# Kernel optimization log

Measured on AMD Instinct MI355X. Metric: run time of the kernel, lower is better.

## Reference

```python
import jax, jax.numpy as jnp
import numpy as np

M, N_IN, K_OUT = 65536, 512, 512  # tokens, in_features, out_features


def setup_inputs() -> dict:
    key = jax.random.key(0)
    k1, k2, k3 = jax.random.split(key, 3)
    X = jax.random.normal(k1, (M, N_IN), dtype=jnp.float32)
    Weight = jax.random.normal(k2, (K_OUT, N_IN), dtype=jnp.float32) * 0.02
    Bias = jax.random.normal(k3, (K_OUT,), dtype=jnp.float32) * 0.02
    return {"X": X, "Weight": Weight, "Bias": Bias}


def reference(X, Weight, Bias):
    # Normalization constants (map X and W into (0,1)-ish analog ranges)
    n_x = jnp.max(X)
    n_w = jnp.maximum(jnp.abs(jnp.min(Weight)), jnp.abs(jnp.max(Weight)))
    X_norm = X / n_x
    W_norm = Weight / n_w
    # quick_split_W3D: W_norm = W_pos - W_neg, each non-negative
    W_pos = jax.nn.relu(W_norm)
    W_neg = jax.nn.relu(-W_norm)
    # Matmul_2D (SIMULATE='False' path): the (m,n,k) Hadamard-product expansion
    # summed over n is exactly X_norm @ W.T; compute the two GEMMs explicitly
    # to preserve the split-weight floating-point path.
    prod_plus = X_norm @ W_pos.T   # (m, k)
    prod_minus = X_norm @ W_neg.T  # (m, k)
    out = n_x * n_w * (prod_plus - prod_minus) + Bias
    return out
```

## Files before the change

### kernel.cpp

```cpp
#include <hip/hip_runtime.h>
#include <hip/hip_bf16.h>


typedef __bf16 bf16x8 __attribute__((ext_vector_type(8)));
typedef float  f32x4  __attribute__((ext_vector_type(4)));

constexpr int M_TOK = 65536;
constexpr int K_IN  = 512;
constexpr int N_OUT = 512;

constexpr int BM = 128, BN = 128, BK = 32;
constexpr int PK = BK + 8;

__global__ __launch_bounds__(256, 2)
void linear_sim_kernel(const float* __restrict__ X,
                       const float* __restrict__ W,
                       const float* __restrict__ Bias,
                       float* __restrict__ Out)
{
    __shared__ __bf16 As[BM][PK];
    __shared__ __bf16 Bs[BN][PK];

    const int bid = blockIdx.x;
    const int nb  = bid & 3;
    const int mb  = bid >> 2;
    const int m0 = mb * BM, n0 = nb * BN;

    const int tid  = threadIdx.x;
    const int lane = tid & 63;
    const int wave = tid >> 6;
    const int wm = wave >> 1;
    const int wn = wave & 1;

    const int srow = tid >> 1;
    const int sk   = (tid & 1) * 16;

    const float* Xp = X + (size_t)(m0 + srow) * K_IN + sk;
    const float* Wp = W + (size_t)(n0 + srow) * K_IN + sk;

    f32x4 acc[16];
    const f32x4 zero = {0.f, 0.f, 0.f, 0.f};
    #pragma unroll
    for (int i = 0; i < 16; ++i) acc[i] = zero;

    const int l15 = lane & 15;
    const int lg  = lane >> 4;

    for (int k0 = 0; k0 < K_IN; k0 += BK) {
        f32x4 xa[4], wb[4];
        #pragma unroll
        for (int q = 0; q < 4; ++q) xa[q] = *(const f32x4*)(Xp + k0 + q * 4);
        #pragma unroll
        for (int q = 0; q < 4; ++q) wb[q] = *(const f32x4*)(Wp + k0 + q * 4);

        __syncthreads();

        #pragma unroll
        for (int h = 0; h < 2; ++h) {
            bf16x8 ta, tb;
            #pragma unroll
            for (int q = 0; q < 2; ++q)
                #pragma unroll
                for (int e = 0; e < 4; ++e) {
                    ta[q * 4 + e] = (__bf16)xa[h * 2 + q][e];
                    tb[q * 4 + e] = (__bf16)wb[h * 2 + q][e];
                }
            *(bf16x8*)&As[srow][sk + h * 8] = ta;
            *(bf16x8*)&Bs[srow][sk + h * 8] = tb;
        }

        __syncthreads();

        bf16x8 af[4], bfr[4];
        #pragma unroll
        for (int i = 0; i < 4; ++i)
            af[i] = *(const bf16x8*)&As[wm * 64 + i * 16 + l15][lg * 8];
        #pragma unroll
        for (int i = 0; i < 4; ++i)
            bfr[i] = *(const bf16x8*)&Bs[wn * 64 + i * 16 + l15][lg * 8];

        #pragma unroll
        for (int mi = 0; mi < 4; ++mi)
            #pragma unroll
            for (int ni = 0; ni < 4; ++ni)
                acc[mi * 4 + ni] = __builtin_amdgcn_mfma_f32_16x16x32_bf16(
                    af[mi], bfr[ni], acc[mi * 4 + ni], 0, 0, 0);
    }

    #pragma unroll
    for (int ni = 0; ni < 4; ++ni) {
        const int col = n0 + wn * 64 + ni * 16 + l15;
        const float bv = Bias[col];
        #pragma unroll
        for (int mi = 0; mi < 4; ++mi) {
            const int row0 = m0 + wm * 64 + mi * 16 + lg * 4;
            f32x4 a = acc[mi * 4 + ni];
            #pragma unroll
            for (int r = 0; r < 4; ++r)
                Out[(size_t)(row0 + r) * N_OUT + col] = a[r] + bv;
        }
    }
}

extern "C" void kernel_launch(void* const* d_in, const int* in_sizes, int n_in,
                              void* d_out, int out_size, void* d_ws, size_t ws_size,
                              hipStream_t stream) {
    const float* X    = (const float*)d_in[0];
    const float* W    = (const float*)d_in[1];
    const float* Bias = (const float*)d_in[2];
    float* Out        = (float*)d_out;

    dim3 grid((M_TOK / BM) * (N_OUT / BN));
    linear_sim_kernel<<<grid, dim3(256), 0, stream>>>(X, W, Bias, Out);
}
```

Before: 305.9 us.

## Double-buffer LDS tiles with register prefetch, XCD-aware block remap, nontemporal stores

Splits the shared-memory tiles into two buffers. The next K-slice is loaded from global memory into registers and written into the alternate buffer after the MFMAs, which cuts the loop from two barriers per step to one and overlaps the loads with compute. It also raises the launch-bounds occupancy hint to 4 blocks per CU. Block indices are remapped so consecutive blocks are spread across XCDs, and the output is written with nontemporal stores. In exchange the LDS footprint doubles and register pressure rises, which could conflict with the higher occupancy target.

```diff
diff --git a/kernel.cpp b/kernel.cpp
--- a/kernel.cpp
+++ b/kernel.cpp
@@ -11,19 +11,21 @@
 
 constexpr int BM = 128, BN = 128, BK = 32;
 constexpr int PK = BK + 8;
+constexpr int NT = K_IN / BK;
 
-__global__ __launch_bounds__(256, 2)
+__global__ __launch_bounds__(256, 4)
 void linear_sim_kernel(const float* __restrict__ X,
                        const float* __restrict__ W,
                        const float* __restrict__ Bias,
                        float* __restrict__ Out)
 {
-    __shared__ __bf16 As[BM][PK];
-    __shared__ __bf16 Bs[BN][PK];
+    __shared__ __bf16 As[2][BM][PK];
+    __shared__ __bf16 Bs[2][BN][PK];
 
-    const int bid = blockIdx.x;
-    const int nb  = bid & 3;
-    const int mb  = bid >> 2;
+    const int d  = blockIdx.x;
+    const int o  = (d & 7) * 256 + (d >> 3);
+    const int nb = o & 3;
+    const int mb = o >> 2;
     const int m0 = mb * BM, n0 = nb * BN;
 
     const int tid  = threadIdx.x;
@@ -46,38 +48,44 @@
     const int l15 = lane & 15;
     const int lg  = lane >> 4;
 
-    for (int k0 = 0; k0 < K_IN; k0 += BK) {
-        f32x4 xa[4], wb[4];
+    f32x4 xa[4], wb[4];
+    #pragma unroll
+    for (int q = 0; q < 4; ++q) xa[q] = *(const f32x4*)(Xp + q * 4);
+    #pragma unroll
+    for (int q = 0; q < 4; ++q) wb[q] = *(const f32x4*)(Wp + q * 4);
+    #pragma unroll
+    for (int h = 0; h < 2; ++h) {
+        bf16x8 ta, tb;
         #pragma unroll
-        for (int q = 0; q < 4; ++q) xa[q] = *(const f32x4*)(Xp + k0 + q * 4);
-        #pragma unroll
-        for (int q = 0; q < 4; ++q) wb[q] = *(const f32x4*)(Wp + k0 + q * 4);
+        for (int q = 0; q < 2; ++q)
+            #pragma unroll
+            for (int e = 0; e < 4; ++e) {
+                ta[q * 4 + e] = (__bf16)xa[h * 2 + q][e];
+                tb[q * 4 + e] = (__bf16)wb[h * 2 + q][e];
+            }
+        *(bf16x8*)&As[0][srow][sk + h * 8] = ta;
+        *(bf16x8*)&Bs[0][srow][sk + h * 8] = tb;
+    }
+    __syncthreads();
 
-        __syncthreads();
-
-        #pragma unroll
-        for (int h = 0; h < 2; ++h) {
-            bf16x8 ta, tb;
+    int cur = 0;
+    for (int t = 0; t < NT; ++t) {
+        const bool pf = (t + 1 < NT);
+        if (pf) {
+            const int k0 = (t + 1) * BK;
             #pragma unroll
-            for (int q = 0; q < 2; ++q)
-                #pragma unroll
-                for (int e = 0; e < 4; ++e) {
-                    ta[q * 4 + e] = (__bf16)xa[h * 2 + q][e];
-                    tb[q * 4 + e] = (__bf16)wb[h * 2 + q][e];
-                }
-            *(bf16x8*)&As[srow][sk + h * 8] = ta;
-            *(bf16x8*)&Bs[srow][sk + h * 8] = tb;
+            for (int q = 0; q < 4; ++q) xa[q] = *(const f32x4*)(Xp + k0 + q * 4);
+            #pragma unroll
+            for (int q = 0; q < 4; ++q) wb[q] = *(const f32x4*)(Wp + k0 + q * 4);
         }
-
-        __syncthreads();
 
         bf16x8 af[4], bfr[4];
         #pragma unroll
         for (int i = 0; i < 4; ++i)
-            af[i] = *(const bf16x8*)&As[wm * 64 + i * 16 + l15][lg * 8];
+            af[i] = *(const bf16x8*)&As[cur][wm * 64 + i * 16 + l15][lg * 8];
         #pragma unroll
         for (int i = 0; i < 4; ++i)
-            bfr[i] = *(const bf16x8*)&Bs[wn * 64 + i * 16 + l15][lg * 8];
+            bfr[i] = *(const bf16x8*)&Bs[cur][wn * 64 + i * 16 + l15][lg * 8];
 
         #pragma unroll
         for (int mi = 0; mi < 4; ++mi)
@@ -85,6 +93,24 @@
             for (int ni = 0; ni < 4; ++ni)
                 acc[mi * 4 + ni] = __builtin_amdgcn_mfma_f32_16x16x32_bf16(
                     af[mi], bfr[ni], acc[mi * 4 + ni], 0, 0, 0);
+
+        if (pf) {
+            #pragma unroll
+            for (int h = 0; h < 2; ++h) {
+                bf16x8 ta, tb;
+                #pragma unroll
+                for (int q = 0; q < 2; ++q)
+                    #pragma unroll
+                    for (int e = 0; e < 4; ++e) {
+                        ta[q * 4 + e] = (__bf16)xa[h * 2 + q][e];
+                        tb[q * 4 + e] = (__bf16)wb[h * 2 + q][e];
+                    }
+                *(bf16x8*)&As[cur ^ 1][srow][sk + h * 8] = ta;
+                *(bf16x8*)&Bs[cur ^ 1][srow][sk + h * 8] = tb;
+            }
+        }
+        __syncthreads();
+        cur ^= 1;
     }
 
     #pragma unroll
@@ -97,7 +123,8 @@
             f32x4 a = acc[mi * 4 + ni];
             #pragma unroll
             for (int r = 0; r < 4; ++r)
-                Out[(size_t)(row0 + r) * N_OUT + col] = a[r] + bv;
+                __builtin_nontemporal_store(a[r] + bv,
+                    &Out[(size_t)(row0 + r) * N_OUT + col]);
         }
     }
 }
```

Result: slower. 328.4 us (+7.4%).

## Stage X tiles via async global-to-LDS loads with double buffering and swizzle

Applied to the files above, without the earlier changes.

Replaces the register-staged bf16 shared-memory tiles with fp32 X tiles copied directly into LDS by global_load_lds, double-buffered so the next tile's copy overlaps the current tile's MFMA work. An XOR swizzle on chunk positions avoids LDS bank conflicts. Weight fragments are now loaded straight from global memory into registers, skipping LDS. The block index is remapped for L2 locality and occupancy is raised to 3 blocks per CU. The trade-offs are a larger fp32 LDS footprint, bf16 conversion on the read side, and redundant weight loads per wave that lean on the cache.

```diff
diff --git a/kernel.cpp b/kernel.cpp
--- a/kernel.cpp
+++ b/kernel.cpp
@@ -10,74 +10,93 @@
 constexpr int N_OUT = 512;
 
 constexpr int BM = 128, BN = 128, BK = 32;
-constexpr int PK = BK + 8;
+constexpr int NT = K_IN / BK;
 
-__global__ __launch_bounds__(256, 2)
+__global__ __launch_bounds__(256, 3)
 void linear_sim_kernel(const float* __restrict__ X,
                        const float* __restrict__ W,
                        const float* __restrict__ Bias,
                        float* __restrict__ Out)
 {
-    __shared__ __bf16 As[BM][PK];
-    __shared__ __bf16 Bs[BN][PK];
+    __shared__ float As[2][BM][BK];
 
-    const int bid = blockIdx.x;
-    const int nb  = bid & 3;
-    const int mb  = bid >> 2;
+    const int d  = blockIdx.x;
+    const int o  = (d & 7) * 256 + (d >> 3);
+    const int nb = o & 3;
+    const int mb = o >> 2;
     const int m0 = mb * BM, n0 = nb * BN;
 
     const int tid  = threadIdx.x;
     const int lane = tid & 63;
-    const int wave = tid >> 6;
-    const int wm = wave >> 1;
-    const int wn = wave & 1;
+    const int w    = tid >> 6;
+    const int wm = w >> 1, wn = w & 1;
+    const int l15 = lane & 15, lg = lane >> 4;
 
-    const int srow = tid >> 1;
-    const int sk   = (tid & 1) * 16;
+    const int lrow8  = lane >> 3;
+    const int gchunk = (lane & 7) ^ lrow8;
 
-    const float* Xp = X + (size_t)(m0 + srow) * K_IN + sk;
-    const float* Wp = W + (size_t)(n0 + srow) * K_IN + sk;
+    const float* Wrow[4];
+    #pragma unroll
+    for (int i = 0; i < 4; ++i)
+        Wrow[i] = W + (size_t)(n0 + wn * 64 + i * 16 + l15) * K_IN + lg * 8;
 
     f32x4 acc[16];
-    const f32x4 zero = {0.f, 0.f, 0.f, 0.f};
     #pragma unroll
-    for (int i = 0; i < 16; ++i) acc[i] = zero;
+    for (int i = 0; i < 16; ++i) acc[i] = (f32x4){0.f, 0.f, 0.f, 0.f};
 
-    const int l15 = lane & 15;
-    const int lg  = lane >> 4;
+    const float* Xbase = X + (size_t)m0 * K_IN;
 
-    for (int k0 = 0; k0 < K_IN; k0 += BK) {
-        f32x4 xa[4], wb[4];
+    auto dma_tile = [&](int t, int b) {
+        const int k0 = t * BK;
         #pragma unroll
-        for (int q = 0; q < 4; ++q) xa[q] = *(const f32x4*)(Xp + k0 + q * 4);
+        for (int j = 0; j < 4; ++j) {
+            const int rbase = (j * 4 + w) * 8;
+            const float* src = Xbase + (size_t)(rbase + lrow8) * K_IN + k0 + gchunk * 4;
+            float* dst = &As[b][rbase][0];
+            __builtin_amdgcn_global_load_lds(
+                (const __attribute__((address_space(1))) void*)src,
+                (__attribute__((address_space(3))) void*)dst, 16, 0, 0);
+        }
+    };
+
+    dma_tile(0, 0);
+    __syncthreads();
+
+    for (int t = 0; t < NT; ++t) {
+        const int cur = t & 1;
+
+        const int k0 = t * BK;
+        f32x4 wbf[8];
         #pragma unroll
-        for (int q = 0; q < 4; ++q) wb[q] = *(const f32x4*)(Wp + k0 + q * 4);
-
-        __syncthreads();
-
-        #pragma unroll
-        for (int h = 0; h < 2; ++h) {
-            bf16x8 ta, tb;
-            #pragma unroll
-            for (int q = 0; q < 2; ++q)
-                #pragma unroll
-                for (int e = 0; e < 4; ++e) {
-                    ta[q * 4 + e] = (__bf16)xa[h * 2 + q][e];
-                    tb[q * 4 + e] = (__bf16)wb[h * 2 + q][e];
-                }
-            *(bf16x8*)&As[srow][sk + h * 8] = ta;
-            *(bf16x8*)&Bs[srow][sk + h * 8] = tb;
+        for (int i = 0; i < 4; ++i) {
+            wbf[i * 2]     = *(const f32x4*)(Wrow[i] + k0);
+            wbf[i * 2 + 1] = *(const f32x4*)(Wrow[i] + k0 + 4);
         }
 
-        __syncthreads();
+        if (t + 1 < NT) dma_tile(t + 1, cur ^ 1);
 
         bf16x8 af[4], bfr[4];
         #pragma unroll
-        for (int i = 0; i < 4; ++i)
-            af[i] = *(const bf16x8*)&As[wm * 64 + i * 16 + l15][lg * 8];
+        for (int mi = 0; mi < 4; ++mi) {
+            const int r  = wm * 64 + mi * 16 + l15;
+            const int rx = l15 & 7;
+            f32x4 c0 = *(const f32x4*)&As[cur][r][((2 * lg)     ^ rx) * 4];
+            f32x4 c1 = *(const f32x4*)&As[cur][r][((2 * lg + 1) ^ rx) * 4];
+            bf16x8 v;
+            #pragma unroll
+            for (int e = 0; e < 4; ++e) { v[e] = (__bf16)c0[e]; v[4 + e] = (__bf16)c1[e]; }
+            af[mi] = v;
+        }
         #pragma unroll
-        for (int i = 0; i < 4; ++i)
-            bfr[i] = *(const bf16x8*)&Bs[wn * 64 + i * 16 + l15][lg * 8];
+        for (int i = 0; i < 4; ++i) {
+            bf16x8 v;
+            #pragma unroll
+            for (int e = 0; e < 4; ++e) {
+                v[e]     = (__bf16)wbf[i * 2][e];
+                v[4 + e] = (__bf16)wbf[i * 2 + 1][e];
+            }
+            bfr[i] = v;
+        }
 
         #pragma unroll
         for (int mi = 0; mi < 4; ++mi)
@@ -85,6 +104,8 @@
             for (int ni = 0; ni < 4; ++ni)
                 acc[mi * 4 + ni] = __builtin_amdgcn_mfma_f32_16x16x32_bf16(
                     af[mi], bfr[ni], acc[mi * 4 + ni], 0, 0, 0);
+
+        __syncthreads();
     }
 
     #pragma unroll
```

Measured after the change: 332.6 us. +8.7%, slower.
